# Optimization experiments

Measured on AMD Instinct MI355X. Metric: run time of the kernel, lower is better.

The kernel has to match this reference:

```python
import jax, jax.numpy as jnp
import numpy as np

NUM_NODES = 50000
NUM_HYPEREDGES = 20000
NNZ = 1600000
IN_DIM = 256
OUT_DIM = 128


def setup_inputs() -> dict:
    key = jax.random.key(0)
    k1, k2, k3, k4, k5 = jax.random.split(key, 5)
    x = jax.random.normal(k1, (NUM_NODES, IN_DIM), dtype=jnp.float32)
    node_idx = jax.random.randint(k2, (NNZ,), 0, NUM_NODES)
    edge_idx = jax.random.randint(k3, (NNZ,), 0, NUM_HYPEREDGES)
    hyperedge_index = jnp.stack([node_idx, edge_idx], axis=0)  # [2, nnz]
    # glorot-style init for HypergraphConv's internal Linear (bias=False)
    scale = np.sqrt(6.0 / (IN_DIM + OUT_DIM)).astype(np.float32)
    lin_weight = jax.random.uniform(k4, (IN_DIM, OUT_DIM), dtype=jnp.float32,
                                    minval=-scale, maxval=scale)
    bias = jnp.zeros((OUT_DIM,), dtype=jnp.float32)
    return {"x_node_features": x, "lin_weight": lin_weight, "bias": bias,
            "hyperedge_index": hyperedge_index}


def reference(x_node_features, lin_weight, bias, hyperedge_index):
    src = hyperedge_index[0]   # node ids   [nnz]
    edge = hyperedge_index[1]  # hyperedge ids [nnz]
    ones = jnp.ones_like(src, dtype=x_node_features.dtype)

    # X Theta
    xw = x_node_features @ lin_weight  # [N, F_out]

    # D^{-1}: node degree (hyperedge weights default to 1)
    deg_n = jax.ops.segment_sum(ones, src, num_segments=NUM_NODES)
    d_inv = jnp.where(deg_n > 0, 1.0 / deg_n, 0.0)
    # B^{-1}: hyperedge cardinality
    deg_e = jax.ops.segment_sum(ones, edge, num_segments=NUM_HYPEREDGES)
    b_inv = jnp.where(deg_e > 0, 1.0 / deg_e, 0.0)

    # node -> hyperedge: m_e = B_e^{-1} * sum_{i in e} (X Theta)_i
    m_e = jax.ops.segment_sum(xw[src], edge, num_segments=NUM_HYPEREDGES)
    m_e = m_e * b_inv[:, None]  # [E, F_out]

    # hyperedge -> node: out_i = D_i^{-1} * sum_{e ni i} m_e
    out = jax.ops.segment_sum(m_e[edge], src, num_segments=NUM_NODES)
    out = out * d_inv[:, None] + bias  # [N, F_out]

    # ReLU + mean pool over nodes
    return jnp.mean(jax.nn.relu(out), axis=0)  # [F_out]
```

## Files before the change

### kernel.cpp

```cpp
#include <hip/hip_runtime.h>

#define NUM_N 50000
#define NUM_E 20000
#define IN_DIM 256
#define OUT_DIM 128
#define NBE 1250
#define NBN 1563
#define NCLS 8
#define ECAPC 256
#define NCAPC 192
#define SCAT_CHUNK 4096
#define NGEMM 782
#define XSCALE 16.0f

typedef unsigned short ushort_t;
typedef unsigned int uint_t;

__device__ __forceinline__ int clamp8(int q) { return min(max(q, -127), 127); }
__device__ __forceinline__ int lo8(uint_t u) { return (int)(signed char)(u & 0xff); }
__device__ __forceinline__ int hi8(uint_t u) { return ((int)(short)(ushort_t)u) >> 8; }

__global__ void init_kernel(int* __restrict__ gcur_e, int* __restrict__ gcur_n,
                            float* __restrict__ macc) {
    int t = blockIdx.x * 1024 + threadIdx.x;
    if (t < NCLS * NBE) gcur_e[t] = t * ECAPC;
    if (t < NCLS * NBN) gcur_n[t] = t * NCAPC;
    if (t < 128) macc[t] = 0.f;
}

__global__ __launch_bounds__(256) void gemm_scatter_kernel(
        const float* __restrict__ x, const float* __restrict__ w,
        char* __restrict__ xw, int nrows,
        const int* __restrict__ node_idx, const int* __restrict__ edge_idx, int nnz,
        int* __restrict__ gcur_e, int* __restrict__ gcur_n,
        uint_t* __restrict__ stag_e, uint_t* __restrict__ stag_n) {
    __shared__ int smem[6208];
    int tid = threadIdx.x;

    if (blockIdx.x >= NGEMM) {
        int* lh    = smem;
        int* lbase = smem + 2813;
        int cls = blockIdx.x & (NCLS - 1);
        int bid = blockIdx.x - NGEMM;
        int nblk = gridDim.x - NGEMM;
        for (int cbase = bid * SCAT_CHUNK; cbase < nnz; cbase += nblk * SCAT_CHUNK) {
            int cend = min(cbase + SCAT_CHUNK, nnz);
            for (int i = tid; i < NBE + NBN; i += 256) lh[i] = 0;
            __syncthreads();
            for (int i = cbase + tid; i < cend; i += 256) {
                atomicAdd(&lh[edge_idx[i] >> 4], 1);
                atomicAdd(&lh[NBE + (node_idx[i] >> 5)], 1);
            }
            __syncthreads();
            for (int i = tid; i < NBE; i += 256) {
                int c = lh[i];
                lbase[i] = c ? atomicAdd(&gcur_e[cls * NBE + i], c) : 0;
            }
            for (int i = tid; i < NBN; i += 256) {
                int c = lh[NBE + i];
                lbase[NBE + i] = c ? atomicAdd(&gcur_n[cls * NBN + i], c) : 0;
            }
            __syncthreads();
            for (int i = tid; i < NBE + NBN; i += 256) lh[i] = 0;
            __syncthreads();
            for (int i = cbase + tid; i < cend; i += 256) {
                int v = node_idx[i];
                int e = edge_idx[i];
                uint_t pk = ((uint_t)v << 16) | (uint_t)e;
                int be = e >> 4;
                int bn = v >> 5;
                int pe = lbase[be] + atomicAdd(&lh[be], 1);
                if (pe < (cls * NBE + be + 1) * ECAPC) stag_e[pe] = pk;
                int pn = lbase[NBE + bn] + atomicAdd(&lh[NBE + bn], 1);
                if (pn < (cls * NBN + bn + 1) * NCAPC) stag_n[pn] = pk;
            }
            __syncthreads();
        }
        return;
    }

    float* As = (float*)smem;
    float* Ws = (float*)smem + 2112;
    int block_row = blockIdx.x * 64;
    int rg = tid >> 4;
    int cg = tid & 15;
    int r0 = rg * 4, c0 = cg * 8;
    float acc[4][8] = {};
    for (int k0 = 0; k0 < IN_DIM; k0 += 32) {
#pragma unroll
        for (int rep = 0; rep < 2; ++rep) {
            int f = tid + rep * 256;
            int row = f >> 3, kq = f & 7;
            float4 v = make_float4(0.f, 0.f, 0.f, 0.f);
            int grow = block_row + row;
            if (grow < nrows) v = *(const float4*)&x[(size_t)grow * IN_DIM + k0 + kq * 4];
            As[row * 33 + kq * 4 + 0] = v.x;
            As[row * 33 + kq * 4 + 1] = v.y;
            As[row * 33 + kq * 4 + 2] = v.z;
            As[row * 33 + kq * 4 + 3] = v.w;
        }
#pragma unroll
        for (int rep = 0; rep < 4; ++rep) {
            int f = tid + rep * 256;
            int kk = f >> 5, cq = f & 31;
            float4 v = *(const float4*)&w[(size_t)(k0 + kk) * OUT_DIM + cq * 4];
            *(float4*)&Ws[kk * 128 + cq * 4] = v;
        }
        __syncthreads();
#pragma unroll
        for (int k = 0; k < 32; ++k) {
            float av[4];
#pragma unroll
            for (int i = 0; i < 4; ++i) av[i] = As[(r0 + i) * 33 + k];
            float4 b0 = *(const float4*)&Ws[k * 128 + c0];
            float4 b1 = *(const float4*)&Ws[k * 128 + c0 + 4];
            float bv[8] = {b0.x, b0.y, b0.z, b0.w, b1.x, b1.y, b1.z, b1.w};
#pragma unroll
            for (int i = 0; i < 4; ++i)
#pragma unroll
                for (int j = 0; j < 8; ++j)
                    acc[i][j] += av[i] * bv[j];
        }
        __syncthreads();
    }
#pragma unroll
    for (int i = 0; i < 4; ++i) {
        int grow = block_row + r0 + i;
        if (grow < nrows) {
            int q[8];
#pragma unroll
            for (int j = 0; j < 8; ++j) q[j] = clamp8(__float2int_rn(acc[i][j] * XSCALE));
            uint2 pk;
            pk.x = (uint_t)(q[0] & 0xff) | ((uint_t)(q[1] & 0xff) << 8) |
                   ((uint_t)(q[2] & 0xff) << 16) | ((uint_t)(q[3] & 0xff) << 24);
            pk.y = (uint_t)(q[4] & 0xff) | ((uint_t)(q[5] & 0xff) << 8) |
                   ((uint_t)(q[6] & 0xff) << 16) | ((uint_t)(q[7] & 0xff) << 24);
            *(uint2*)&xw[(size_t)grow * OUT_DIM + c0] = pk;
        }
    }
}

__global__ __launch_bounds__(256) void edge_agg_kernel(const uint_t* __restrict__ stag_e,
                                                       const int* __restrict__ gcur_e,
                                                       const ushort_t* __restrict__ xw16,
                                                       ushort_t* __restrict__ me16) {
    __shared__ int acc[16 * 128];
    __shared__ int cnt[16];
    int tid = threadIdx.x;
    int lane = tid & 63;
    int wid = tid >> 6;
    int b = blockIdx.x;
    for (int i = tid; i < 16 * 128; i += 256) acc[i] = 0;
    if (tid < 16) cnt[tid] = 0;
    __syncthreads();
    for (int cls = 0; cls < NCLS; ++cls) {
        int idx = cls * NBE + b;
        int beg = idx * ECAPC;
        int end = min(gcur_e[idx], beg + ECAPC);
        int cb = beg + wid * 16;
        for (; cb + 16 <= end; cb += 64) {
            uint4 pa = *(const uint4*)&stag_e[cb];
            uint4 pb = *(const uint4*)&stag_e[cb + 4];
            uint4 pc = *(const uint4*)&stag_e[cb + 8];
            uint4 pd = *(const uint4*)&stag_e[cb + 12];
            uint_t pk[16] = {pa.x, pa.y, pa.z, pa.w, pb.x, pb.y, pb.z, pb.w,
                             pc.x, pc.y, pc.z, pc.w, pd.x, pd.y, pd.z, pd.w};
            uint_t u[16];
#pragma unroll
            for (int j = 0; j < 16; ++j)
                u[j] = xw16[(size_t)(pk[j] >> 16) * 64 + lane];
#pragma unroll
            for (int j = 0; j < 16; ++j) {
                int r = (pk[j] & 15) * 128;
                atomicAdd(&acc[r + lane],      lo8(u[j]));
                atomicAdd(&acc[r + 64 + lane], hi8(u[j]));
            }
            if (lane == 0) {
#pragma unroll
                for (int j = 0; j < 16; ++j) atomicAdd(&cnt[pk[j] & 15], 1);
            }
        }
        if (cb < end) {
            int m = end - cb;
            uint4 pa = *(const uint4*)&stag_e[cb];
            uint4 pb = *(const uint4*)&stag_e[cb + 4];
            uint4 pc = *(const uint4*)&stag_e[cb + 8];
            uint4 pd = *(const uint4*)&stag_e[cb + 12];
            uint_t pk[16] = {pa.x, pa.y, pa.z, pa.w, pb.x, pb.y, pb.z, pb.w,
                             pc.x, pc.y, pc.z, pc.w, pd.x, pd.y, pd.z, pd.w};
            uint_t u[16];
#pragma unroll
            for (int j = 0; j < 16; ++j)
                u[j] = xw16[(size_t)(pk[j] >> 16) * 64 + lane];
#pragma unroll
            for (int j = 0; j < 16; ++j) {
                bool ok = j < m;
                int r = (pk[j] & 15) * 128;
                atomicAdd(&acc[r + lane],      ok ? lo8(u[j]) : 0);
                atomicAdd(&acc[r + 64 + lane], ok ? hi8(u[j]) : 0);
            }
            if (lane == 0) {
#pragma unroll
                for (int j = 0; j < 16; ++j)
                    if (j < m) atomicAdd(&cnt[pk[j] & 15], 1);
            }
        }
    }
    __syncthreads();
    for (int r = wid; r < 16; r += 4) {
        int e = b * 16 + r;
        int c = cnt[r];
        float f = c ? 4.0f / (float)c : 0.f;
        int q0 = clamp8(__float2int_rn((float)acc[r * 128 + lane] * f));
        int q1 = clamp8(__float2int_rn((float)acc[r * 128 + 64 + lane] * f));
        me16[(size_t)e * 64 + lane] = (ushort_t)((q0 & 0xff) | ((q1 & 0xff) << 8));
    }
}

__global__ __launch_bounds__(256) void node_agg_kernel(const uint_t* __restrict__ stag_n,
                                                       const int* __restrict__ gcur_n,
                                                       const ushort_t* __restrict__ me16,
                                                       const float* __restrict__ bias,
                                                       float* __restrict__ mean_acc) {
    __shared__ int acc[32 * 128];
    __shared__ int cnt[32];
    int tid = threadIdx.x;
    int lane = tid & 63;
    int wid = tid >> 6;
    int b = blockIdx.x;
    for (int i = tid; i < 32 * 128; i += 256) acc[i] = 0;
    if (tid < 32) cnt[tid] = 0;
    __syncthreads();
    for (int cls = 0; cls < NCLS; ++cls) {
        int idx = cls * NBN + b;
        int beg = idx * NCAPC;
        int end = min(gcur_n[idx], beg + NCAPC);
        int cb = beg + wid * 16;
        for (; cb + 16 <= end; cb += 64) {
            uint4 pa = *(const uint4*)&stag_n[cb];
            uint4 pb = *(const uint4*)&stag_n[cb + 4];
            uint4 pc = *(const uint4*)&stag_n[cb + 8];
            uint4 pd = *(const uint4*)&stag_n[cb + 12];
            uint_t pk[16] = {pa.x, pa.y, pa.z, pa.w, pb.x, pb.y, pb.z, pb.w,
                             pc.x, pc.y, pc.z, pc.w, pd.x, pd.y, pd.z, pd.w};
            uint_t u[16];
#pragma unroll
            for (int j = 0; j < 16; ++j)
                u[j] = me16[(size_t)(pk[j] & 0xffff) * 64 + lane];
#pragma unroll
            for (int j = 0; j < 16; ++j) {
                int r = ((pk[j] >> 16) & 31) * 128;
                atomicAdd(&acc[r + lane],      lo8(u[j]));
                atomicAdd(&acc[r + 64 + lane], hi8(u[j]));
            }
            if (lane == 0) {
#pragma unroll
                for (int j = 0; j < 16; ++j) atomicAdd(&cnt[(pk[j] >> 16) & 31], 1);
            }
        }
        if (cb < end) {
            int m = end - cb;
            uint4 pa = *(const uint4*)&stag_n[cb];
            uint4 pb = *(const uint4*)&stag_n[cb + 4];
            uint4 pc = *(const uint4*)&stag_n[cb + 8];
            uint4 pd = *(const uint4*)&stag_n[cb + 12];
            uint_t pk[16] = {pa.x, pa.y, pa.z, pa.w, pb.x, pb.y, pb.z, pb.w,
                             pc.x, pc.y, pc.z, pc.w, pd.x, pd.y, pd.z, pd.w};
            uint_t u[16];
#pragma unroll
            for (int j = 0; j < 16; ++j)
                u[j] = me16[(size_t)(pk[j] & 0xffff) * 64 + lane];
#pragma unroll
            for (int j = 0; j < 16; ++j) {
                bool ok = j < m;
                int r = ((pk[j] >> 16) & 31) * 128;
                atomicAdd(&acc[r + lane],      ok ? lo8(u[j]) : 0);
                atomicAdd(&acc[r + 64 + lane], ok ? hi8(u[j]) : 0);
            }
            if (lane == 0) {
#pragma unroll
                for (int j = 0; j < 16; ++j)
                    if (j < m) atomicAdd(&cnt[(pk[j] >> 16) & 31], 1);
            }
        }
    }
    __syncthreads();
    if (tid < 128) {
        int c = tid;
        int sw = (c & 1) ? (64 + (c >> 1)) : (c >> 1);
        float bc = bias[c];
        float s = 0.f;
        int nmax = min(32, NUM_N - b * 32);
        for (int r = 0; r < nmax; ++r) {
            int cc = cnt[r];
            float dinv = cc ? 1.0f / (64.0f * (float)cc) : 0.f;
            s += fmaxf((float)acc[r * 128 + sw] * dinv + bc, 0.f);
        }
        atomicAdd(&mean_acc[c], s);
    }
}

__global__ void finalize_kernel(const float* __restrict__ mean_acc, float* __restrict__ out) {
    int t = threadIdx.x;
    if (t < 128) out[t] = mean_acc[t] * (1.0f / (float)NUM_N);
}

extern "C" void kernel_launch(void* const* d_in, const int* in_sizes, int n_in,
                              void* d_out, int out_size, void* d_ws, size_t ws_size,
                              hipStream_t stream) {
    const float* x    = (const float*)d_in[0];
    const float* w    = (const float*)d_in[1];
    const float* bias = (const float*)d_in[2];
    const int*   hei  = (const int*)d_in[3];
    int nnz = in_sizes[3] / 2;
    const int* node_idx = hei;
    const int* edge_idx = hei + nnz;
    float* out = (float*)d_out;

    char* ws = (char*)d_ws;
    char*     xw     = ws;
    ushort_t* me16   = (ushort_t*)(ws + 6400000);
    uint_t*   stag_e = (uint_t*)(ws + 8960000);
    uint_t*   stag_n = (uint_t*)(ws + 19200064);
    int* gcur_e = (int*)(ws + 28803200);
    int* gcur_n = (int*)(ws + 28843200);
    float* macc = (float*)(ws + 28893216);

    int nscat = (nnz + SCAT_CHUNK - 1) / SCAT_CHUNK;

    init_kernel<<<13, 1024, 0, stream>>>(gcur_e, gcur_n, macc);
    gemm_scatter_kernel<<<NGEMM + nscat, 256, 0, stream>>>(
        x, w, xw, NUM_N, node_idx, edge_idx, nnz, gcur_e, gcur_n, stag_e, stag_n);

    edge_agg_kernel<<<NBE, 256, 0, stream>>>(stag_e, gcur_e, (const ushort_t*)xw, me16);
    node_agg_kernel<<<NBN, 256, 0, stream>>>(stag_n, gcur_n, me16, bias, macc);
    finalize_kernel<<<1, 128, 0, stream>>>(macc, out);
}
```

Baseline: 208.2 us.

## Use bf16 MFMA for the X*W GEMM instead of scalar FP32 FMA

Replaces the shared-memory tiled FP32 FMA GEMM with a wave-level bf16 MFMA (16x16x32) path. Each wave computes 16 rows by 128 output columns, loading its A fragment straight from global memory and converting it to bf16. W is transposed into LDS as bf16 on every k-step. This reduces the GEMM's compute cost but lowers input precision to bf16, and the int8 output is now written as single-byte scattered stores instead of packed 8-byte stores.

```diff
diff --git a/kernel.cpp b/kernel.cpp
--- a/kernel.cpp
+++ b/kernel.cpp
@@ -15,10 +15,17 @@
 
 typedef unsigned short ushort_t;
 typedef unsigned int uint_t;
+typedef __attribute__((ext_vector_type(8))) short short8_t;
+typedef __attribute__((ext_vector_type(4))) float f32x4_t;
 
 __device__ __forceinline__ int clamp8(int q) { return min(max(q, -127), 127); }
 __device__ __forceinline__ int lo8(uint_t u) { return (int)(signed char)(u & 0xff); }
 __device__ __forceinline__ int hi8(uint_t u) { return ((int)(short)(ushort_t)u) >> 8; }
+__device__ __forceinline__ ushort_t f2bf(float f) {
+    uint_t u = __float_as_uint(f);
+    u += 0x7fffu + ((u >> 16) & 1u);
+    return (ushort_t)(u >> 16);
+}
 
 __global__ void init_kernel(int* __restrict__ gcur_e, int* __restrict__ gcur_n,
                             float* __restrict__ macc) {
@@ -34,7 +41,7 @@
         const int* __restrict__ node_idx, const int* __restrict__ edge_idx, int nnz,
         int* __restrict__ gcur_e, int* __restrict__ gcur_n,
         uint_t* __restrict__ stag_e, uint_t* __restrict__ stag_n) {
-    __shared__ int smem[6208];
+    __shared__ int smem[5632];
     int tid = threadIdx.x;
 
     if (blockIdx.x >= NGEMM) {
@@ -79,63 +86,57 @@
         return;
     }
 
-    float* As = (float*)smem;
-    float* Ws = (float*)smem + 2112;
-    int block_row = blockIdx.x * 64;
-    int rg = tid >> 4;
-    int cg = tid & 15;
-    int r0 = rg * 4, c0 = cg * 8;
-    float acc[4][8] = {};
+    ushort_t* Wt = (ushort_t*)smem;
+    int lane = tid & 63;
+    int wv = tid >> 6;
+    int R = blockIdx.x * 64 + wv * 16;
+    int fr = lane & 15;
+    int kb = lane >> 4;
+    f32x4_t acc[8];
+#pragma unroll
+    for (int c = 0; c < 8; ++c) acc[c] = (f32x4_t){0.f, 0.f, 0.f, 0.f};
+    int arow = min(R + fr, nrows - 1);
+    const float* ap = x + (size_t)arow * IN_DIM + kb * 8;
+
     for (int k0 = 0; k0 < IN_DIM; k0 += 32) {
-#pragma unroll
-        for (int rep = 0; rep < 2; ++rep) {
-            int f = tid + rep * 256;
-            int row = f >> 3, kq = f & 7;
-            float4 v = make_float4(0.f, 0.f, 0.f, 0.f);
-            int grow = block_row + row;
-            if (grow < nrows) v = *(const float4*)&x[(size_t)grow * IN_DIM + k0 + kq * 4];
-            As[row * 33 + kq * 4 + 0] = v.x;
-            As[row * 33 + kq * 4 + 1] = v.y;
-            As[row * 33 + kq * 4 + 2] = v.z;
-            As[row * 33 + kq * 4 + 3] = v.w;
-        }
-#pragma unroll
-        for (int rep = 0; rep < 4; ++rep) {
-            int f = tid + rep * 256;
-            int kk = f >> 5, cq = f & 31;
-            float4 v = *(const float4*)&w[(size_t)(k0 + kk) * OUT_DIM + cq * 4];
-            *(float4*)&Ws[kk * 128 + cq * 4] = v;
-        }
         __syncthreads();
-#pragma unroll
-        for (int k = 0; k < 32; ++k) {
-            float av[4];
-#pragma unroll
-            for (int i = 0; i < 4; ++i) av[i] = As[(r0 + i) * 33 + k];
-            float4 b0 = *(const float4*)&Ws[k * 128 + c0];
-            float4 b1 = *(const float4*)&Ws[k * 128 + c0 + 4];
-            float bv[8] = {b0.x, b0.y, b0.z, b0.w, b1.x, b1.y, b1.z, b1.w};
-#pragma unroll
-            for (int i = 0; i < 4; ++i)
-#pragma unroll
-                for (int j = 0; j < 8; ++j)
-                    acc[i][j] += av[i] * bv[j];
+        {
+            int tk = tid >> 3;
+            int tc = (tid & 7) * 16;
+            const float* wp = w + (size_t)(k0 + tk) * OUT_DIM + tc;
+            float4 w0 = *(const float4*)(wp + 0);
+            float4 w1 = *(const float4*)(wp + 4);
+            float4 w2 = *(const float4*)(wp + 8);
+            float4 w3 = *(const float4*)(wp + 12);
+            float wvv[16] = {w0.x, w0.y, w0.z, w0.w, w1.x, w1.y, w1.z, w1.w,
+                             w2.x, w2.y, w2.z, w2.w, w3.x, w3.y, w3.z, w3.w};
+#pragma unroll
+            for (int i = 0; i < 16; ++i)
+                Wt[(tc + i) * 40 + tk] = f2bf(wvv[i]);
         }
         __syncthreads();
-    }
-#pragma unroll
-    for (int i = 0; i < 4; ++i) {
-        int grow = block_row + r0 + i;
-        if (grow < nrows) {
-            int q[8];
-#pragma unroll
-            for (int j = 0; j < 8; ++j) q[j] = clamp8(__float2int_rn(acc[i][j] * XSCALE));
-            uint2 pk;
-            pk.x = (uint_t)(q[0] & 0xff) | ((uint_t)(q[1] & 0xff) << 8) |
-                   ((uint_t)(q[2] & 0xff) << 16) | ((uint_t)(q[3] & 0xff) << 24);
-            pk.y = (uint_t)(q[4] & 0xff) | ((uint_t)(q[5] & 0xff) << 8) |
-                   ((uint_t)(q[6] & 0xff) << 16) | ((uint_t)(q[7] & 0xff) << 24);
-            *(uint2*)&xw[(size_t)grow * OUT_DIM + c0] = pk;
+        float4 a0 = *(const float4*)(ap + k0);
+        float4 a1 = *(const float4*)(ap + k0 + 4);
+        short8_t af;
+        af[0] = (short)f2bf(a0.x); af[1] = (short)f2bf(a0.y);
+        af[2] = (short)f2bf(a0.z); af[3] = (short)f2bf(a0.w);
+        af[4] = (short)f2bf(a1.x); af[5] = (short)f2bf(a1.y);
+        af[6] = (short)f2bf(a1.z); af[7] = (short)f2bf(a1.w);
+#pragma unroll
+        for (int c = 0; c < 8; ++c) {
+            short8_t bf = *(short8_t*)&Wt[(c * 16 + fr) * 40 + kb * 8];
+            acc[c] = __builtin_amdgcn_mfma_f32_16x16x32_bf16(af, bf, acc[c], 0, 0, 0);
+        }
+    }
+#pragma unroll
+    for (int c = 0; c < 8; ++c) {
+#pragma unroll
+        for (int j = 0; j < 4; ++j) {
+            int row = R + kb * 4 + j;
+            if (row < nrows) {
+                int q = clamp8(__float2int_rn(acc[c][j] * XSCALE));
+                xw[(size_t)row * OUT_DIM + c * 16 + fr] = (char)q;
+            }
         }
     }
 }
```

Result: faster. 196.9 us (-5.5%).
